# Kernel optimization log

Measured on AMD Instinct MI355X. Metric: run time of the kernel, lower is better.

## Reference

```python
import jax, jax.numpy as jnp
import numpy as np

N_QUBITS = 4
N_LAYERS = 2
FS = 2          # filter_size
STRIDE = 1
DIM = 2 ** N_QUBITS  # 16

# mean over qubits of PauliZ eigenvalue per computational-basis state
_idx = np.arange(DIM)
_bits = np.stack([(_idx >> (N_QUBITS - 1 - q)) & 1 for q in range(N_QUBITS)], 0)  # [4,16]
Z_MEAN = jnp.asarray((1.0 - 2.0 * _bits).mean(0), dtype=jnp.float32)               # [16]


def ry_mat(t):
    c, s = jnp.cos(t / 2), jnp.sin(t / 2)
    m = jnp.stack([jnp.stack([c, -s], -1), jnp.stack([s, c], -1)], -2)
    return m.astype(jnp.complex64)


def rx_mat(t):
    c = jnp.cos(t / 2).astype(jnp.complex64)
    s = (jnp.sin(t / 2) * (-1j)).astype(jnp.complex64)
    return jnp.stack([jnp.stack([c, s], -1), jnp.stack([s, c], -1)], -2)


def rz_mat(t):
    e = jnp.exp((t / 2).astype(jnp.complex64) * (-1j))
    z = jnp.zeros_like(e)
    return jnp.stack([jnp.stack([e, z], -1), jnp.stack([z, jnp.conj(e)], -1)], -2)


def apply_1q(state, U, q):
    # state: [N,2,2,2,2] complex; U: [2,2] or batched [N,2,2]
    st = jnp.moveaxis(state, 1 + q, -1)
    if U.ndim == 3:
        st = jnp.einsum('nab,n...b->n...a', U, st)
    else:
        st = jnp.einsum('ab,n...b->n...a', U, st)
    return jnp.moveaxis(st, -1, 1 + q)


def apply_cnot(state, c, t):
    st = jnp.moveaxis(state, (1 + c, 1 + t), (-2, -1))
    st = jnp.stack([st[..., 0, :], st[..., 1, ::-1]], axis=-2)
    return jnp.moveaxis(st, (-2, -1), (1 + c, 1 + t))


def apply_cry(state, theta, c, t):
    U = ry_mat(theta)
    st = jnp.moveaxis(state, (1 + c, 1 + t), (-2, -1))
    bot = jnp.einsum('ab,n...b->n...a', U, st[..., 1, :])
    st = jnp.stack([st[..., 0, :], bot], axis=-2)
    return jnp.moveaxis(st, (-2, -1), (1 + c, 1 + t))


def _forward(x, weights):
    B, H, W, C = x.shape
    oh = (H - FS) // STRIDE + 1
    ow = (W - FS) // STRIDE + 1
    # extract all patches at once: [B, oh, ow, FS, FS, C]
    ri = (jnp.arange(oh) * STRIDE)[:, None, None, None] + jnp.arange(FS)[None, None, :, None]
    ci = (jnp.arange(ow) * STRIDE)[None, :, None, None] + jnp.arange(FS)[None, None, None, :]
    patches = x[:, ri, ci, :]
    pf = patches.reshape(B * oh * ow, FS * FS * C)
    # tf.nn.l2_normalize over the whole (flat) patch, eps=1e-12
    norm = pf * jax.lax.rsqrt(jnp.maximum(jnp.sum(pf * pf, -1, keepdims=True), 1e-12))
    ang = norm[:, :N_QUBITS]  # RY angles, [N,4]
    N = pf.shape[0]

    # |0000> encoded state, batched over all patches
    state = jnp.zeros((N, DIM), jnp.complex64).at[:, 0].set(1.0)
    state = state.reshape((N,) + (2,) * N_QUBITS)
    for q in range(N_QUBITS):
        state = apply_1q(state, ry_mat(ang[:, q]), q)
    for q in range(N_QUBITS - 1):
        state = apply_cnot(state, q, q + 1)

    outs = []
    for f in range(weights.shape[0]):
        w = weights[f]
        s = state
        for layer in range(N_LAYERS):
            base = layer * N_QUBITS * 3
            for q in range(N_QUBITS):
                p = base + q * 3
                s = apply_1q(s, rx_mat(w[p]), q)
                s = apply_1q(s, ry_mat(w[p + 1]), q)
                s = apply_1q(s, rz_mat(w[p + 2]), q)
            # CRY on even pairs, reusing weights[base + i] (as in the source)
            for q in range(0, N_QUBITS - 1, 2):
                s = apply_cry(s, w[base + q], q, q + 1)
        sf = s.reshape(N, DIM)
        probs = jnp.real(sf * jnp.conj(sf))           # [N,16]
        outs.append((probs @ Z_MEAN).reshape(B, oh, ow))  # mean of <Z_q>
    return jnp.stack(outs, -1)  # [B, oh, ow, n_filters]


def setup_inputs() -> dict:
    key = jax.random.key(0)
    k1, k2 = jax.random.split(key)
    x = jax.random.normal(k1, (8, 96, 96, 16), dtype=jnp.float32)
    # keras 'random_uniform' initializer default range
    weights = jax.random.uniform(k2, (8, 24), dtype=jnp.float32, minval=-0.05, maxval=0.05)
    return {"x": x, "weights": weights}


def reference(x, weights):
    return _forward(x, weights)
```

## Files before the change

kernel.cpp:

```cpp
#include <hip/hip_runtime.h>

namespace {
constexpr int DIM = 16;
constexpr int BATCH = 8;
constexpr int H = 96, W = 96, CH = 16;
constexpr int OH = 95, OW = 95;
constexpr int NF = 8, NW = 24;
constexpr int NPIX = BATCH * OH * OW;
constexpr int PBLK = (NPIX + 255) / 256;
constexpr int PSI_OFF = NF * 512;
}

__global__ void build_u_kernel(const float* __restrict__ wts, float* __restrict__ ws) {
  const int f = blockIdx.x;
  const int col = threadIdx.x;
  const float* w = wts + f * NW;

  float ar[DIM], ai[DIM];
#pragma unroll
  for (int i = 0; i < DIM; ++i) { ar[i] = (i == col) ? 1.f : 0.f; ai[i] = 0.f; }

#pragma unroll
  for (int layer = 0; layer < 2; ++layer) {
    const int wb = layer * 12;
#pragma unroll
    for (int q = 0; q < 4; ++q) {
      const int m = 8 >> q;
      float c, s;
      {
        __sincosf(w[wb + q * 3] * 0.5f, &s, &c);
#pragma unroll
        for (int i = 0; i < DIM; ++i) {
          if (i & m) continue;
          const int j = i | m;
          const float a0r = ar[i], a0i = ai[i], a1r = ar[j], a1i = ai[j];
          ar[i] = fmaf(c, a0r,  s * a1i);
          ai[i] = fmaf(c, a0i, -s * a1r);
          ar[j] = fmaf(c, a1r,  s * a0i);
          ai[j] = fmaf(c, a1i, -s * a0r);
        }
      }
      {
        __sincosf(w[wb + q * 3 + 1] * 0.5f, &s, &c);
#pragma unroll
        for (int i = 0; i < DIM; ++i) {
          if (i & m) continue;
          const int j = i | m;
          const float a0r = ar[i], a0i = ai[i], a1r = ar[j], a1i = ai[j];
          ar[i] = fmaf(c, a0r, -s * a1r);
          ai[i] = fmaf(c, a0i, -s * a1i);
          ar[j] = fmaf(s, a0r,  c * a1r);
          ai[j] = fmaf(s, a0i,  c * a1i);
        }
      }
      {
        __sincosf(w[wb + q * 3 + 2] * 0.5f, &s, &c);
#pragma unroll
        for (int i = 0; i < DIM; ++i) {
          const float r = ar[i], im = ai[i];
          if (i & m) { ar[i] = fmaf(c, r, -s * im); ai[i] = fmaf(c, im,  s * r); }
          else       { ar[i] = fmaf(c, r,  s * im); ai[i] = fmaf(c, im, -s * r); }
        }
      }
    }
    {
      float c, s;
      __sincosf(w[wb + 0] * 0.5f, &s, &c);
#pragma unroll
      for (int i = 0; i < DIM; ++i) {
        if (!(i & 8) || (i & 4)) continue;
        const int j = i | 4;
        const float a0r = ar[i], a0i = ai[i], a1r = ar[j], a1i = ai[j];
        ar[i] = fmaf(c, a0r, -s * a1r);
        ai[i] = fmaf(c, a0i, -s * a1i);
        ar[j] = fmaf(s, a0r,  c * a1r);
        ai[j] = fmaf(s, a0i,  c * a1i);
      }
    }
    {
      float c, s;
      __sincosf(w[wb + 2] * 0.5f, &s, &c);
#pragma unroll
      for (int i = 0; i < DIM; ++i) {
        if (!(i & 2) || (i & 1)) continue;
        const int j = i | 1;
        const float a0r = ar[i], a0i = ai[i], a1r = ar[j], a1i = ai[j];
        ar[i] = fmaf(c, a0r, -s * a1r);
        ai[i] = fmaf(c, a0i, -s * a1i);
        ar[j] = fmaf(s, a0r,  c * a1r);
        ai[j] = fmaf(s, a0i,  c * a1i);
      }
    }
  }

  float* dst = ws + f * 512 + col * 32;
#pragma unroll
  for (int i = 0; i < DIM; ++i) { dst[i] = ar[i]; dst[16 + i] = ai[i]; }
}

__global__ __launch_bounds__(256)
void psi_kernel(const float* __restrict__ x, float* __restrict__ ws) {
  const int n = blockIdx.x * 256 + threadIdx.x;
  if (n >= NPIX) return;
  const int b = n / (OH * OW);
  const int rem = n - b * (OH * OW);
  const int oi = rem / OW;
  const int oj = rem - oi * OW;

  const float* base = x + (((b * H) + oi) * W + oj) * CH;
  float ss = 0.f;
  float4 f0 = make_float4(0.f, 0.f, 0.f, 0.f);
#pragma unroll
  for (int fi = 0; fi < 2; ++fi) {
    const float4* row = reinterpret_cast<const float4*>(base + fi * W * CH);
#pragma unroll
    for (int k = 0; k < 8; ++k) {
      const float4 v = row[k];
      if (fi == 0 && k == 0) f0 = v;
      ss = fmaf(v.x, v.x, ss); ss = fmaf(v.y, v.y, ss);
      ss = fmaf(v.z, v.z, ss); ss = fmaf(v.w, v.w, ss);
    }
  }
  const float inv = rsqrtf(fmaxf(ss, 1e-12f));

  float cq[4], sq[4];
  __sincosf(f0.x * inv * 0.5f, &sq[0], &cq[0]);
  __sincosf(f0.y * inv * 0.5f, &sq[1], &cq[1]);
  __sincosf(f0.z * inv * 0.5f, &sq[2], &cq[2]);
  __sincosf(f0.w * inv * 0.5f, &sq[3], &cq[3]);

  float st[DIM];
#pragma unroll
  for (int i = 0; i < DIM; ++i) {
    const float pr = ((i & 8) ? sq[0] : cq[0]) * ((i & 4) ? sq[1] : cq[1]) *
                     ((i & 2) ? sq[2] : cq[2]) * ((i & 1) ? sq[3] : cq[3]);
    int j = i;
    if (j & 8) j ^= 4;
    if (j & 4) j ^= 2;
    if (j & 2) j ^= 1;
    st[j] = pr;
  }

  float4* dst = reinterpret_cast<float4*>(ws + PSI_OFF + n * 16);
  dst[0] = make_float4(st[0], st[1], st[2], st[3]);
  dst[1] = make_float4(st[4], st[5], st[6], st[7]);
  dst[2] = make_float4(st[8], st[9], st[10], st[11]);
  dst[3] = make_float4(st[12], st[13], st[14], st[15]);
}

__global__ __launch_bounds__(256)
void apply_kernel(const float* __restrict__ ws, float* __restrict__ out) {
  __shared__ float U[512];
  const int tid = threadIdx.x;
  const int f = blockIdx.y;
  if (tid < 128)
    reinterpret_cast<float4*>(U)[tid] =
        reinterpret_cast<const float4*>(ws + f * 512)[tid];
  __syncthreads();

  const int n = blockIdx.x * 256 + tid;
  const bool valid = n < NPIX;
  const int nc = valid ? n : NPIX - 1;

  float psi[DIM];
  {
    const float4* pp = reinterpret_cast<const float4*>(ws + PSI_OFF + nc * 16);
    const float4 a = pp[0], b4 = pp[1], c4 = pp[2], d4 = pp[3];
    psi[0] = a.x;  psi[1] = a.y;  psi[2] = a.z;  psi[3] = a.w;
    psi[4] = b4.x; psi[5] = b4.y; psi[6] = b4.z; psi[7] = b4.w;
    psi[8] = c4.x; psi[9] = c4.y; psi[10] = c4.z; psi[11] = c4.w;
    psi[12] = d4.x; psi[13] = d4.y; psi[14] = d4.z; psi[15] = d4.w;
  }

  float yr[DIM], yi[DIM];
#pragma unroll
  for (int i = 0; i < DIM; ++i) { yr[i] = 0.f; yi[i] = 0.f; }

  const float4* l4 = reinterpret_cast<const float4*>(U);
#define FMA4(dst, d0, v)                      \
  dst[d0 + 0] = fmaf((v).x, pk, dst[d0 + 0]); \
  dst[d0 + 1] = fmaf((v).y, pk, dst[d0 + 1]); \
  dst[d0 + 2] = fmaf((v).z, pk, dst[d0 + 2]); \
  dst[d0 + 3] = fmaf((v).w, pk, dst[d0 + 3]);
#pragma unroll
  for (int k = 0; k < DIM; ++k) {
    const float pk = psi[k];
    const float4 r0 = l4[k * 8 + 0], r1 = l4[k * 8 + 1];
    const float4 r2 = l4[k * 8 + 2], r3 = l4[k * 8 + 3];
    const float4 i0 = l4[k * 8 + 4], i1 = l4[k * 8 + 5];
    const float4 i2 = l4[k * 8 + 6], i3 = l4[k * 8 + 7];
    FMA4(yr, 0, r0) FMA4(yr, 4, r1) FMA4(yr, 8, r2) FMA4(yr, 12, r3)
    FMA4(yi, 0, i0) FMA4(yi, 4, i1) FMA4(yi, 8, i2) FMA4(yi, 12, i3)
  }
#undef FMA4

  float p[DIM];
#pragma unroll
  for (int i = 0; i < DIM; ++i) p[i] = fmaf(yr[i], yr[i], yi[i] * yi[i]);
  const float acc = (p[0] - p[15]) +
                    0.5f * ((p[1] + p[2] + p[4] + p[8]) -
                            (p[7] + p[11] + p[13] + p[14]));
  if (valid) out[nc * NF + f] = acc;
}

extern "C" void kernel_launch(void* const* d_in, const int* in_sizes, int n_in,
                              void* d_out, int out_size, void* d_ws, size_t ws_size,
                              hipStream_t stream) {
  const float* x = (const float*)d_in[0];
  const float* w = (const float*)d_in[1];
  float* out = (float*)d_out;
  float* ws = (float*)d_ws;

  build_u_kernel<<<dim3(NF), dim3(DIM), 0, stream>>>(w, ws);
  psi_kernel<<<dim3(PBLK), dim3(256), 0, stream>>>(x, ws);
  apply_kernel<<<dim3(PBLK, NF), dim3(256), 0, stream>>>(ws, out);
}
```

Before: 85.78 us.

## Fold unitary and Z observable into real quadratic form; merge prep kernels

Because the input state is real, the expectation psi^T Re(U^H Z U) psi can use a precomputed real symmetric 16x16 matrix per filter, with the CNOT-like permutation folded into the matrix indices. This replaces the complex matvec plus probability step with a real matvec and a dot product, roughly halving arithmetic per pixel-filter. Building the unitaries and the psi vectors now happens in one kernel (an extra block computes the matrices), which removes a launch. The apply kernel maps all 8 filters of 32 pixels into each block, so writes become coalesced and psi is shared across filters, with padded LDS rows.

```diff
diff --git a/kernel.cpp b/kernel.cpp
--- a/kernel.cpp
+++ b/kernel.cpp
@@ -7,200 +7,239 @@
 constexpr int OH = 95, OW = 95;
 constexpr int NF = 8, NW = 24;
 constexpr int NPIX = BATCH * OH * OW;
-constexpr int PBLK = (NPIX + 255) / 256;
-constexpr int PSI_OFF = NF * 512;
-}
-
-__global__ void build_u_kernel(const float* __restrict__ wts, float* __restrict__ ws) {
-  const int f = blockIdx.x;
-  const int col = threadIdx.x;
-  const float* w = wts + f * NW;
-
-  float ar[DIM], ai[DIM];
-#pragma unroll
-  for (int i = 0; i < DIM; ++i) { ar[i] = (i == col) ? 1.f : 0.f; ai[i] = 0.f; }
-
-#pragma unroll
-  for (int layer = 0; layer < 2; ++layer) {
-    const int wb = layer * 12;
-#pragma unroll
-    for (int q = 0; q < 4; ++q) {
-      const int m = 8 >> q;
-      float c, s;
-      {
-        __sincosf(w[wb + q * 3] * 0.5f, &s, &c);
+constexpr int PSIBLK = (NPIX + 255) / 256;
+constexpr int M_FLOATS = NF * 256;
+constexpr int PSI_OFF = M_FLOATS;
+constexpr int PPB = 32;
+constexpr int APBLK = (NPIX + PPB - 1) / PPB;
+constexpr int MPAD = 260;
+}
+
+__device__ __forceinline__ int permf(int i) {
+  int j = i;
+  if (j & 8) j ^= 4;
+  if (j & 4) j ^= 2;
+  if (j & 2) j ^= 1;
+  return j;
+}
+
+__global__ __launch_bounds__(256)
+void prep_kernel(const float* __restrict__ x, const float* __restrict__ wts,
+                 float* __restrict__ ws) {
+  const int tid = threadIdx.x;
+  if (blockIdx.x == PSIBLK) {
+    __shared__ float ur[NF * 256];
+    __shared__ float ui[NF * 256];
+    const int f = tid >> 4;
+    const int col = tid & 15;
+    if (tid < NF * DIM) {
+      const float* w = wts + f * NW;
+      float ar[DIM], ai[DIM];
+#pragma unroll
+      for (int i = 0; i < DIM; ++i) { ar[i] = (i == col) ? 1.f : 0.f; ai[i] = 0.f; }
+#pragma unroll
+      for (int layer = 0; layer < 2; ++layer) {
+        const int wb = layer * 12;
+#pragma unroll
+        for (int q = 0; q < 4; ++q) {
+          const int m = 8 >> q;
+          float c, s;
+          {
+            __sincosf(w[wb + q * 3] * 0.5f, &s, &c);
+#pragma unroll
+            for (int i = 0; i < DIM; ++i) {
+              if (i & m) continue;
+              const int j = i | m;
+              const float a0r = ar[i], a0i = ai[i], a1r = ar[j], a1i = ai[j];
+              ar[i] = fmaf(c, a0r,  s * a1i);
+              ai[i] = fmaf(c, a0i, -s * a1r);
+              ar[j] = fmaf(c, a1r,  s * a0i);
+              ai[j] = fmaf(c, a1i, -s * a0r);
+            }
+          }
+          {
+            __sincosf(w[wb + q * 3 + 1] * 0.5f, &s, &c);
+#pragma unroll
+            for (int i = 0; i < DIM; ++i) {
+              if (i & m) continue;
+              const int j = i | m;
+              const float a0r = ar[i], a0i = ai[i], a1r = ar[j], a1i = ai[j];
+              ar[i] = fmaf(c, a0r, -s * a1r);
+              ai[i] = fmaf(c, a0i, -s * a1i);
+              ar[j] = fmaf(s, a0r,  c * a1r);
+              ai[j] = fmaf(s, a0i,  c * a1i);
+            }
+          }
+          {
+            __sincosf(w[wb + q * 3 + 2] * 0.5f, &s, &c);
+#pragma unroll
+            for (int i = 0; i < DIM; ++i) {
+              const float r = ar[i], im = ai[i];
+              if (i & m) { ar[i] = fmaf(c, r, -s * im); ai[i] = fmaf(c, im,  s * r); }
+              else       { ar[i] = fmaf(c, r,  s * im); ai[i] = fmaf(c, im, -s * r); }
+            }
+          }
+        }
+        {
+          float c, s;
+          __sincosf(w[wb + 0] * 0.5f, &s, &c);
+#pragma unroll
+          for (int i = 0; i < DIM; ++i) {
+            if (!(i & 8) || (i & 4)) continue;
+            const int j = i | 4;
+            const float a0r = ar[i], a0i = ai[i], a1r = ar[j], a1i = ai[j];
+            ar[i] = fmaf(c, a0r, -s * a1r);
+            ai[i] = fmaf(c, a0i, -s * a1i);
+            ar[j] = fmaf(s, a0r,  c * a1r);
+            ai[j] = fmaf(s, a0i,  c * a1i);
+          }
+        }
+        {
+          float c, s;
+          __sincosf(w[wb + 2] * 0.5f, &s, &c);
+#pragma unroll
+          for (int i = 0; i < DIM; ++i) {
+            if (!(i & 2) || (i & 1)) continue;
+            const int j = i | 1;
+            const float a0r = ar[i], a0i = ai[i], a1r = ar[j], a1i = ai[j];
+            ar[i] = fmaf(c, a0r, -s * a1r);
+            ai[i] = fmaf(c, a0i, -s * a1i);
+            ar[j] = fmaf(s, a0r,  c * a1r);
+            ai[j] = fmaf(s, a0i,  c * a1i);
+          }
+        }
+      }
+#pragma unroll
+      for (int i = 0; i < DIM; ++i) {
+        ur[f * 256 + col * 16 + i] = ar[i];
+        ui[f * 256 + col * 16 + i] = ai[i];
+      }
+    }
+    __syncthreads();
+    if (tid < NF * DIM) {
+      const int k = col;
+      const int pk = permf(k);
+      const float* cr = ur + f * 256;
+      const float* ci = ui + f * 256;
+      float* dst = ws + f * 256 + k * 16;
+#pragma unroll
+      for (int j = 0; j < DIM; ++j) {
+        const int pj = permf(j);
+        float acc = 0.f;
 #pragma unroll
         for (int i = 0; i < DIM; ++i) {
-          if (i & m) continue;
-          const int j = i | m;
-          const float a0r = ar[i], a0i = ai[i], a1r = ar[j], a1i = ai[j];
-          ar[i] = fmaf(c, a0r,  s * a1i);
-          ai[i] = fmaf(c, a0i, -s * a1r);
-          ar[j] = fmaf(c, a1r,  s * a0i);
-          ai[j] = fmaf(c, a1i, -s * a0r);
-        }
-      }
-      {
-        __sincosf(w[wb + q * 3 + 1] * 0.5f, &s, &c);
-#pragma unroll
-        for (int i = 0; i < DIM; ++i) {
-          if (i & m) continue;
-          const int j = i | m;
-          const float a0r = ar[i], a0i = ai[i], a1r = ar[j], a1i = ai[j];
-          ar[i] = fmaf(c, a0r, -s * a1r);
-          ai[i] = fmaf(c, a0i, -s * a1i);
-          ar[j] = fmaf(s, a0r,  c * a1r);
-          ai[j] = fmaf(s, a0i,  c * a1i);
-        }
-      }
-      {
-        __sincosf(w[wb + q * 3 + 2] * 0.5f, &s, &c);
-#pragma unroll
-        for (int i = 0; i < DIM; ++i) {
-          const float r = ar[i], im = ai[i];
-          if (i & m) { ar[i] = fmaf(c, r, -s * im); ai[i] = fmaf(c, im,  s * r); }
-          else       { ar[i] = fmaf(c, r,  s * im); ai[i] = fmaf(c, im, -s * r); }
-        }
-      }
-    }
-    {
-      float c, s;
-      __sincosf(w[wb + 0] * 0.5f, &s, &c);
-#pragma unroll
-      for (int i = 0; i < DIM; ++i) {
-        if (!(i & 8) || (i & 4)) continue;
-        const int j = i | 4;
-        const float a0r = ar[i], a0i = ai[i], a1r = ar[j], a1i = ai[j];
-        ar[i] = fmaf(c, a0r, -s * a1r);
-        ai[i] = fmaf(c, a0i, -s * a1i);
-        ar[j] = fmaf(s, a0r,  c * a1r);
-        ai[j] = fmaf(s, a0i,  c * a1i);
-      }
-    }
-    {
-      float c, s;
-      __sincosf(w[wb + 2] * 0.5f, &s, &c);
-#pragma unroll
-      for (int i = 0; i < DIM; ++i) {
-        if (!(i & 2) || (i & 1)) continue;
-        const int j = i | 1;
-        const float a0r = ar[i], a0i = ai[i], a1r = ar[j], a1i = ai[j];
-        ar[i] = fmaf(c, a0r, -s * a1r);
-        ai[i] = fmaf(c, a0i, -s * a1i);
-        ar[j] = fmaf(s, a0r,  c * a1r);
-        ai[j] = fmaf(s, a0i,  c * a1i);
-      }
-    }
-  }
-
-  float* dst = ws + f * 512 + col * 32;
-#pragma unroll
-  for (int i = 0; i < DIM; ++i) { dst[i] = ar[i]; dst[16 + i] = ai[i]; }
-}
-
-__global__ __launch_bounds__(256)
-void psi_kernel(const float* __restrict__ x, float* __restrict__ ws) {
-  const int n = blockIdx.x * 256 + threadIdx.x;
-  if (n >= NPIX) return;
-  const int b = n / (OH * OW);
-  const int rem = n - b * (OH * OW);
-  const int oi = rem / OW;
-  const int oj = rem - oi * OW;
-
-  const float* base = x + (((b * H) + oi) * W + oj) * CH;
-  float ss = 0.f;
-  float4 f0 = make_float4(0.f, 0.f, 0.f, 0.f);
-#pragma unroll
-  for (int fi = 0; fi < 2; ++fi) {
-    const float4* row = reinterpret_cast<const float4*>(base + fi * W * CH);
-#pragma unroll
-    for (int k = 0; k < 8; ++k) {
-      const float4 v = row[k];
-      if (fi == 0 && k == 0) f0 = v;
-      ss = fmaf(v.x, v.x, ss); ss = fmaf(v.y, v.y, ss);
-      ss = fmaf(v.z, v.z, ss); ss = fmaf(v.w, v.w, ss);
-    }
-  }
-  const float inv = rsqrtf(fmaxf(ss, 1e-12f));
-
-  float cq[4], sq[4];
-  __sincosf(f0.x * inv * 0.5f, &sq[0], &cq[0]);
-  __sincosf(f0.y * inv * 0.5f, &sq[1], &cq[1]);
-  __sincosf(f0.z * inv * 0.5f, &sq[2], &cq[2]);
-  __sincosf(f0.w * inv * 0.5f, &sq[3], &cq[3]);
-
-  float st[DIM];
-#pragma unroll
-  for (int i = 0; i < DIM; ++i) {
-    const float pr = ((i & 8) ? sq[0] : cq[0]) * ((i & 4) ? sq[1] : cq[1]) *
-                     ((i & 2) ? sq[2] : cq[2]) * ((i & 1) ? sq[3] : cq[3]);
-    int j = i;
-    if (j & 8) j ^= 4;
-    if (j & 4) j ^= 2;
-    if (j & 2) j ^= 1;
-    st[j] = pr;
-  }
-
-  float4* dst = reinterpret_cast<float4*>(ws + PSI_OFF + n * 16);
-  dst[0] = make_float4(st[0], st[1], st[2], st[3]);
-  dst[1] = make_float4(st[4], st[5], st[6], st[7]);
-  dst[2] = make_float4(st[8], st[9], st[10], st[11]);
-  dst[3] = make_float4(st[12], st[13], st[14], st[15]);
+          const float z = 1.f - 0.5f * (float)__popc(i);
+          acc += z * (cr[pk * 16 + i] * cr[pj * 16 + i] +
+                      ci[pk * 16 + i] * ci[pj * 16 + i]);
+        }
+        dst[j] = acc;
+      }
+    }
+  } else {
+    const int n = blockIdx.x * 256 + tid;
+    if (n >= NPIX) return;
+    const int b = n / (OH * OW);
+    const int rem = n - b * (OH * OW);
+    const int oi = rem / OW;
+    const int oj = rem - oi * OW;
+
+    const float* base = x + (((b * H) + oi) * W + oj) * CH;
+    float ss = 0.f;
+    float4 f0 = make_float4(0.f, 0.f, 0.f, 0.f);
+#pragma unroll
+    for (int fi = 0; fi < 2; ++fi) {
+      const float4* row = reinterpret_cast<const float4*>(base + fi * W * CH);
+#pragma unroll
+      for (int k = 0; k < 8; ++k) {
+        const float4 v = row[k];
+        if (fi == 0 && k == 0) f0 = v;
+        ss = fmaf(v.x, v.x, ss); ss = fmaf(v.y, v.y, ss);
+        ss = fmaf(v.z, v.z, ss); ss = fmaf(v.w, v.w, ss);
+      }
+    }
+    const float inv = rsqrtf(fmaxf(ss, 1e-12f));
+
+    float cq[4], sq[4];
+    __sincosf(f0.x * inv * 0.5f, &sq[0], &cq[0]);
+    __sincosf(f0.y * inv * 0.5f, &sq[1], &cq[1]);
+    __sincosf(f0.z * inv * 0.5f, &sq[2], &cq[2]);
+    __sincosf(f0.w * inv * 0.5f, &sq[3], &cq[3]);
+
+    float st[DIM];
+#pragma unroll
+    for (int i = 0; i < DIM; ++i) {
+      st[i] = ((i & 8) ? sq[0] : cq[0]) * ((i & 4) ? sq[1] : cq[1]) *
+              ((i & 2) ? sq[2] : cq[2]) * ((i & 1) ? sq[3] : cq[3]);
+    }
+    float4* dst = reinterpret_cast<float4*>(ws + PSI_OFF + n * 16);
+    dst[0] = make_float4(st[0], st[1], st[2], st[3]);
+    dst[1] = make_float4(st[4], st[5], st[6], st[7]);
+    dst[2] = make_float4(st[8], st[9], st[10], st[11]);
+    dst[3] = make_float4(st[12], st[13], st[14], st[15]);
+  }
 }
 
 __global__ __launch_bounds__(256)
 void apply_kernel(const float* __restrict__ ws, float* __restrict__ out) {
-  __shared__ float U[512];
+  __shared__ float M[NF * MPAD];
   const int tid = threadIdx.x;
-  const int f = blockIdx.y;
-  if (tid < 128)
-    reinterpret_cast<float4*>(U)[tid] =
-        reinterpret_cast<const float4*>(ws + f * 512)[tid];
+#pragma unroll
+  for (int it = 0; it < 2; ++it) {
+    const int i = it * 256 + tid;
+    const int ff = i >> 6;
+    const int r = i & 63;
+    reinterpret_cast<float4*>(M + ff * MPAD)[r] =
+        reinterpret_cast<const float4*>(ws)[i];
+  }
   __syncthreads();
 
-  const int n = blockIdx.x * 256 + tid;
+  const int p = tid >> 3;
+  const int f = tid & 7;
+  const int n = blockIdx.x * PPB + p;
   const bool valid = n < NPIX;
   const int nc = valid ? n : NPIX - 1;
 
   float psi[DIM];
   {
     const float4* pp = reinterpret_cast<const float4*>(ws + PSI_OFF + nc * 16);
-    const float4 a = pp[0], b4 = pp[1], c4 = pp[2], d4 = pp[3];
-    psi[0] = a.x;  psi[1] = a.y;  psi[2] = a.z;  psi[3] = a.w;
-    psi[4] = b4.x; psi[5] = b4.y; psi[6] = b4.z; psi[7] = b4.w;
-    psi[8] = c4.x; psi[9] = c4.y; psi[10] = c4.z; psi[11] = c4.w;
-    psi[12] = d4.x; psi[13] = d4.y; psi[14] = d4.z; psi[15] = d4.w;
-  }
-
-  float yr[DIM], yi[DIM];
-#pragma unroll
-  for (int i = 0; i < DIM; ++i) { yr[i] = 0.f; yi[i] = 0.f; }
-
-  const float4* l4 = reinterpret_cast<const float4*>(U);
-#define FMA4(dst, d0, v)                      \
-  dst[d0 + 0] = fmaf((v).x, pk, dst[d0 + 0]); \
-  dst[d0 + 1] = fmaf((v).y, pk, dst[d0 + 1]); \
-  dst[d0 + 2] = fmaf((v).z, pk, dst[d0 + 2]); \
-  dst[d0 + 3] = fmaf((v).w, pk, dst[d0 + 3]);
+    const float4 a0 = pp[0], a1 = pp[1], a2 = pp[2], a3 = pp[3];
+    psi[0] = a0.x;  psi[1] = a0.y;  psi[2] = a0.z;  psi[3] = a0.w;
+    psi[4] = a1.x;  psi[5] = a1.y;  psi[6] = a1.z;  psi[7] = a1.w;
+    psi[8] = a2.x;  psi[9] = a2.y;  psi[10] = a2.z; psi[11] = a2.w;
+    psi[12] = a3.x; psi[13] = a3.y; psi[14] = a3.z; psi[15] = a3.w;
+  }
+
+  float yv[DIM];
+#pragma unroll
+  for (int i = 0; i < DIM; ++i) yv[i] = 0.f;
+
+  const float4* mrow = reinterpret_cast<const float4*>(M + f * MPAD);
 #pragma unroll
   for (int k = 0; k < DIM; ++k) {
-    const float pk = psi[k];
-    const float4 r0 = l4[k * 8 + 0], r1 = l4[k * 8 + 1];
-    const float4 r2 = l4[k * 8 + 2], r3 = l4[k * 8 + 3];
-    const float4 i0 = l4[k * 8 + 4], i1 = l4[k * 8 + 5];
-    const float4 i2 = l4[k * 8 + 6], i3 = l4[k * 8 + 7];
-    FMA4(yr, 0, r0) FMA4(yr, 4, r1) FMA4(yr, 8, r2) FMA4(yr, 12, r3)
-    FMA4(yi, 0, i0) FMA4(yi, 4, i1) FMA4(yi, 8, i2) FMA4(yi, 12, i3)
-  }
-#undef FMA4
-
-  float p[DIM];
-#pragma unroll
-  for (int i = 0; i < DIM; ++i) p[i] = fmaf(yr[i], yr[i], yi[i] * yi[i]);
-  const float acc = (p[0] - p[15]) +
-                    0.5f * ((p[1] + p[2] + p[4] + p[8]) -
-                            (p[7] + p[11] + p[13] + p[14]));
-  if (valid) out[nc * NF + f] = acc;
+    const float t = psi[k];
+    const float4 m0 = mrow[k * 4 + 0];
+    const float4 m1 = mrow[k * 4 + 1];
+    const float4 m2 = mrow[k * 4 + 2];
+    const float4 m3 = mrow[k * 4 + 3];
+    yv[0]  = fmaf(m0.x, t, yv[0]);  yv[1]  = fmaf(m0.y, t, yv[1]);
+    yv[2]  = fmaf(m0.z, t, yv[2]);  yv[3]  = fmaf(m0.w, t, yv[3]);
+    yv[4]  = fmaf(m1.x, t, yv[4]);  yv[5]  = fmaf(m1.y, t, yv[5]);
+    yv[6]  = fmaf(m1.z, t, yv[6]);  yv[7]  = fmaf(m1.w, t, yv[7]);
+    yv[8]  = fmaf(m2.x, t, yv[8]);  yv[9]  = fmaf(m2.y, t, yv[9]);
+    yv[10] = fmaf(m2.z, t, yv[10]); yv[11] = fmaf(m2.w, t, yv[11]);
+    yv[12] = fmaf(m3.x, t, yv[12]); yv[13] = fmaf(m3.y, t, yv[13]);
+    yv[14] = fmaf(m3.z, t, yv[14]); yv[15] = fmaf(m3.w, t, yv[15]);
+  }
+
+  float s0 = 0.f, s1 = 0.f, s2 = 0.f, s3 = 0.f;
+#pragma unroll
+  for (int i = 0; i < DIM; i += 4) {
+    s0 = fmaf(psi[i + 0], yv[i + 0], s0);
+    s1 = fmaf(psi[i + 1], yv[i + 1], s1);
+    s2 = fmaf(psi[i + 2], yv[i + 2], s2);
+    s3 = fmaf(psi[i + 3], yv[i + 3], s3);
+  }
+  if (valid) out[blockIdx.x * 256 + tid] = (s0 + s1) + (s2 + s3);
 }
 
 extern "C" void kernel_launch(void* const* d_in, const int* in_sizes, int n_in,
@@ -211,7 +250,6 @@
   float* out = (float*)d_out;
   float* ws = (float*)d_ws;
 
-  build_u_kernel<<<dim3(NF), dim3(DIM), 0, stream>>>(w, ws);
-  psi_kernel<<<dim3(PBLK), dim3(256), 0, stream>>>(x, ws);
-  apply_kernel<<<dim3(PBLK, NF), dim3(256), 0, stream>>>(ws, out);
-}
+  prep_kernel<<<dim3(PSIBLK + 1), dim3(256), 0, stream>>>(x, w, ws);
+  apply_kernel<<<dim3(APBLK), dim3(256), 0, stream>>>(ws, out);
+}
```

After: 78.03 us. 1.1x faster.
